# Performance work log

Measured on AMD Instinct MI355X. Metric: run time of the kernel, lower is better.

The kernel has to match this reference:

```python
import jax, jax.numpy as jnp
import numpy as np

B, S, D, H = 2, 2048, 1024, 16
DK = D // H
DFF = 4 * D
EPS = 1e-6


def layer_norm(x, gamma, beta):
    mu = jnp.mean(x, axis=-1, keepdims=True)
    var = jnp.mean(jnp.square(x - mu), axis=-1, keepdims=True)
    return (x - mu) * jax.lax.rsqrt(var + EPS) * gamma + beta


def setup_inputs() -> dict:
    key = jax.random.key(0)
    ks = jax.random.split(key, 10)
    xavier = (6.0 / (D + D)) ** 0.5
    kaiming = (6.0 / D) ** 0.5
    kaiming2 = (6.0 / DFF) ** 0.5
    return {
        "batch_X": jax.random.normal(ks[0], (B, S, D), dtype=jnp.float32),
        "padding_mask": jax.random.randint(ks[1], (B, S), 0, 2, dtype=jnp.int32),
        "W_Q": jax.random.uniform(ks[2], (D, D), jnp.float32, -xavier, xavier),
        "W_K": jax.random.uniform(ks[3], (D, D), jnp.float32, -xavier, xavier),
        "W_V": jax.random.uniform(ks[4], (D, D), jnp.float32, -xavier, xavier),
        "W_O": jax.random.uniform(ks[5], (D, D), jnp.float32, -xavier, xavier),
        "W1": jax.random.uniform(ks[6], (D, DFF), jnp.float32, -kaiming, kaiming),
        "b1": jnp.zeros((DFF,), jnp.float32),
        "W2": jax.random.uniform(ks[7], (DFF, D), jnp.float32, -kaiming2, kaiming2),
        "b2": jnp.zeros((D,), jnp.float32),
        "gamma1": jnp.ones((D,), jnp.float32),
        "beta1": jnp.zeros((D,), jnp.float32),
        "gamma2": jnp.ones((D,), jnp.float32),
        "beta2": jnp.zeros((D,), jnp.float32),
    }


def reference(batch_X, padding_mask, W_Q, W_K, W_V, W_O, W1, b1, W2, b2,
              gamma1, beta1, gamma2, beta2):
    x = batch_X
    b, s, d = x.shape

    # --- multi-head self-attention (use_mask=False: padding mask only) ---
    q = (x @ W_Q).reshape(b, s, H, DK)
    k = (x @ W_K).reshape(b, s, H, DK)
    v = (x @ W_V).reshape(b, s, H, DK)
    scores = jnp.einsum("bqhd,bkhd->bhqk", q, k) / jnp.sqrt(jnp.float32(DK))
    # mask[b,i,j] = (padding_mask[b,i] == 0) for all j: whole query rows are
    # either fully masked (softmax -> NaN -> zeroed in the original) or
    # fully unmasked. Equivalent math: softmax then zero padded query rows.
    probs = jax.nn.softmax(scores, axis=-1)
    keep = (padding_mask != 0).astype(probs.dtype)[:, None, :, None]  # [B,1,S,1]
    probs = probs * keep
    ctx = jnp.einsum("bhqk,bkhd->bqhd", probs, v).reshape(b, s, d)
    attn_out = ctx @ W_O

    # --- residual + LN (dropout identity in eval) ---
    x = x + layer_norm(attn_out, gamma1, beta1)

    # --- FFN ---
    h = jax.nn.relu(x @ W1 + b1)
    ffn_out = h @ W2 + b2
    x = x + layer_norm(ffn_out, gamma2, beta2)
    return x
```

## Files before the change

kernel.cpp:

```cpp
#include <hip/hip_runtime.h>

#define B 2
#define S 2048
#define D 1024
#define H 16
#define DKh 64
#define DFF 4096
#define M (B*S)

typedef unsigned short u16;
typedef unsigned int u32;
typedef __attribute__((ext_vector_type(8))) short short8;
typedef __attribute__((ext_vector_type(4))) float f32x4;

__device__ __forceinline__ u16 f2bf(float f) {
  union { float f; unsigned u; } v; v.f = f;
  unsigned r = v.u + 0x7fffu + ((v.u >> 16) & 1u);
  return (u16)(r >> 16);
}

__device__ __forceinline__ u32 pkbf(float a, float b) {
  union { float f; u32 u; } ua, ub; ua.f = a; ub.f = b;
  return ((ub.u + 0x8000u) & 0xffff0000u) | ((ua.u + 0x8000u) >> 16);
}

__device__ __forceinline__ void gload16(const void* g, void* l) {
  __builtin_amdgcn_global_load_lds((const __attribute__((address_space(1))) void*)g,
                                   (__attribute__((address_space(3))) void*)l, 16, 0, 0);
}

#define SBAR()  __builtin_amdgcn_sched_barrier(0)
#define WBAR()  __builtin_amdgcn_s_barrier()

__global__ __launch_bounds__(256) void cvtbf(const float* __restrict__ in,
                                             u16* __restrict__ out, int n4) {
  int i = blockIdx.x * 256 + threadIdx.x;
  if (i >= n4) return;
  float4 v = ((const float4*)in)[i];
  ushort4 o = make_ushort4(f2bf(v.x), f2bf(v.y), f2bf(v.z), f2bf(v.w));
  ((ushort4*)out)[i] = o;
}

__global__ __launch_bounds__(256) void tcvt(const float* __restrict__ W,
                                            u16* __restrict__ Wt, int K, int N) {
  __shared__ u16 l[64][65];
  const int n0 = blockIdx.x * 64, k0 = blockIdx.y * 64;
  const int tx = threadIdx.x & 63, ty = threadIdx.x >> 6;
#pragma unroll
  for (int j = 0; j < 16; ++j) {
    int r = j * 4 + ty;
    l[r][tx] = f2bf(W[(size_t)(k0 + r) * N + n0 + tx]);
  }
  __syncthreads();
#pragma unroll
  for (int j = 0; j < 16; ++j) {
    int r = j * 4 + ty;
    Wt[(size_t)(n0 + r) * K + k0 + tx] = l[tx][r];
  }
}

__global__ __launch_bounds__(256) void vtrans(const u16* __restrict__ V,
                                              u16* __restrict__ Vt, int ld) {
  __shared__ u16 l[64][65];
  const int s0 = blockIdx.x * 64, by = blockIdx.y;
  const int b = by >> 4, h = by & 15;
  const int tx = threadIdx.x & 63, ty = threadIdx.x >> 6;
#pragma unroll
  for (int j = 0; j < 16; ++j) {
    int r = j * 4 + ty;
    l[r][tx] = V[(size_t)(b * S + s0 + r) * ld + h * DKh + tx];
  }
  __syncthreads();
#pragma unroll
  for (int j = 0; j < 16; ++j) {
    int r = j * 4 + ty;
    Vt[(size_t)(by * 64 + r) * S + s0 + tx] = l[tx][r];
  }
}

template<int EPI>
__global__ __launch_bounds__(512, 2) void gemm256(const u16* __restrict__ Ag,
    const u16* __restrict__ Bg, void* __restrict__ Cout,
    const float* __restrict__ bias, int Mm, int N, int ld, int Kper) {
  __shared__ u16 lA[2 * 16384];
  __shared__ u16 lB[2 * 16384];
  const int t = threadIdx.x;
  const int lane = t & 63, w = t >> 6;
  const int wm = w >> 2, wn = w & 3;
  const int g = lane >> 4, c = lane & 15;
  const int swz = (c & 7) << 4;

  const int gx = gridDim.x, gy = gridDim.y;
  const int orig = blockIdx.y * gx + blockIdx.x;
  const int qchunk = (gx * gy) >> 3;
  const int wg = (orig & 7) * qchunk + (orig >> 3);
  const int bn0 = (wg % gx) * 256, bm0 = (wg / gx) * 256;
  const int koff = blockIdx.z * Kper;
  const int nk = Kper >> 6;

  f32x4 acc[8][4] = {};
  short8 af[4][2], bf[2][2];

  auto stageA = [&](int h, int buf, int kt) {
#pragma unroll
    for (int i = 0; i < 2; ++i) {
      int chunk = i * 512 + t;
      int rh = chunk >> 3;
      int cb = (chunk & 7) * 16;
      int r = (rh & 63) + (h + 2 * (rh >> 6)) * 64;
      gload16(Ag + (size_t)(bm0 + r) * ld + koff + kt * 64 + ((cb ^ ((r & 7) << 4)) >> 1),
              (void*)((char*)lA + buf * 32768 + h * 16384 + chunk * 16));
    }
  };
  auto stageB = [&](int h, int buf, int kt) {
#pragma unroll
    for (int i = 0; i < 2; ++i) {
      int chunk = i * 512 + t;
      int rh = chunk >> 3;
      int cb = (chunk & 7) * 16;
      int r = (rh & 31) + (h + 2 * (rh >> 5)) * 32;
      gload16(Bg + (size_t)(bn0 + r) * ld + koff + kt * 64 + ((cb ^ ((r & 7) << 4)) >> 1),
              (void*)((char*)lB + buf * 32768 + h * 16384 + chunk * 16));
    }
  };

#define RDA(mh) { const char* lab = (const char*)lA + cur * 32768;                          \
  _Pragma("unroll") for (int mt2 = 0; mt2 < 4; ++mt2)                                       \
    _Pragma("unroll") for (int kc = 0; kc < 2; ++kc)                                        \
      af[mt2][kc] = *(const short8*)(lab + (wm * 64 + (mh) * 128 + mt2 * 16 + c) * 128      \
                                         + ((kc * 64 + g * 16) ^ swz)); }
#define RDB(nh) { const char* lbb = (const char*)lB + cur * 32768;                          \
  _Pragma("unroll") for (int nt2 = 0; nt2 < 2; ++nt2)                                       \
    _Pragma("unroll") for (int kc = 0; kc < 2; ++kc)                                        \
      bf[nt2][kc] = *(const short8*)(lbb + ((nh) * 128 + wn * 32 + nt2 * 16 + c) * 128      \
                                         + ((kc * 64 + g * 16) ^ swz)); }
#define QMFMA(mh, nh) { __builtin_amdgcn_s_setprio(1);                                      \
  _Pragma("unroll") for (int mt2 = 0; mt2 < 4; ++mt2)                                       \
    _Pragma("unroll") for (int nt2 = 0; nt2 < 2; ++nt2)                                     \
      _Pragma("unroll") for (int kc = 0; kc < 2; ++kc)                                      \
        acc[(mh) * 4 + mt2][(nh) * 2 + nt2] = __builtin_amdgcn_mfma_f32_16x16x32_bf16(      \
            af[mt2][kc], bf[nt2][kc], acc[(mh) * 4 + mt2][(nh) * 2 + nt2], 0, 0, 0);        \
  __builtin_amdgcn_s_setprio(0); }

  stageA(0, 0, 0); stageB(0, 0, 0); stageA(1, 0, 0); stageB(1, 0, 0);
  asm volatile("s_waitcnt vmcnt(4)" ::: "memory");
  SBAR(); WBAR(); SBAR();

  int cur = 0;
  for (int kt = 0; kt < nk; ++kt) {
    const bool more = (kt + 1 < nk);
    RDB(0); RDA(0);
    if (more) { stageA(0, cur ^ 1, kt + 1);
                asm volatile("s_waitcnt vmcnt(4)" ::: "memory"); }
    else      { asm volatile("s_waitcnt vmcnt(2)" ::: "memory"); }
    SBAR(); WBAR(); SBAR();
    QMFMA(0, 0);
    SBAR(); WBAR(); SBAR();
    RDA(1);
    if (more) { stageB(0, cur ^ 1, kt + 1);
                asm volatile("s_waitcnt vmcnt(4)" ::: "memory"); }
    else      { asm volatile("s_waitcnt vmcnt(0)" ::: "memory"); }
    SBAR(); WBAR(); SBAR();
    QMFMA(1, 0);
    SBAR(); WBAR(); SBAR();
    RDB(1);
    if (more) stageA(1, cur ^ 1, kt + 1);
    SBAR(); WBAR(); SBAR();
    QMFMA(1, 1);
    SBAR(); WBAR(); SBAR();
    RDA(0);
    if (more) { stageB(1, cur ^ 1, kt + 1);
                asm volatile("s_waitcnt vmcnt(4)" ::: "memory"); }
    SBAR(); WBAR(); SBAR();
    QMFMA(0, 1);
    SBAR(); WBAR(); SBAR();
    cur ^= 1;
  }
#undef RDA
#undef RDB
#undef QMFMA

  float* plane = (EPI == 1) ? ((float*)Cout + (size_t)blockIdx.z * Mm * N) : (float*)Cout;
#pragma unroll
  for (int mt = 0; mt < 8; ++mt) {
#pragma unroll
    for (int nt = 0; nt < 4; ++nt) {
      const int col = bn0 + wn * 64 + nt * 16 + c;
      float bv = (EPI == 2) ? bias[col] : 0.0f;
#pragma unroll
      for (int r = 0; r < 4; ++r) {
        const int row = bm0 + wm * 128 + mt * 16 + g * 4 + r;
        float v = acc[mt][nt][r];
        if (EPI == 2) v = fmaxf(v + bv, 0.0f);
        if (EPI == 1) plane[(size_t)row * N + col] = v;
        else          ((u16*)Cout)[(size_t)row * N + col] = f2bf(v);
      }
    }
  }
}

__global__ __launch_bounds__(256) void attn_kernel(const u16* __restrict__ Q,
    const u16* __restrict__ Kp, const u16* __restrict__ Vt,
    const int* __restrict__ mask, u16* __restrict__ Ctx, int ldq) {
  __shared__ u16 lK[2][64 * 64];
  __shared__ u16 lV[2][64 * 64];
  __shared__ u16 lP[4 * 16 * 64];
  const int t = threadIdx.x, lane = t & 63, w = t >> 6;
  const int g = lane >> 4, c = lane & 15;
  const int gx = gridDim.x;
  const int orig = blockIdx.y * gx + blockIdx.x;
  const int qchunk = (gx * gridDim.y) >> 3;
  const int wg = (orig & 7) * qchunk + (orig >> 3);
  const int bx = wg % gx, by = wg / gx;
  const int b = by >> 4, h = by & 15;
  const int q0w = bx * 64 + w * 16;
  const float SCL = 0.18033688011112042f;

  short8 qf[2];
#pragma unroll
  for (int kc = 0; kc < 2; ++kc)
    qf[kc] = *(const short8*)&Q[(size_t)(b * S + q0w + c) * ldq + h * DKh + kc * 32 + g * 8];

  float lsum = 0.0f;
  f32x4 accO[4] = {};

  auto stage = [&](int buf, int it) {
    const int kv0 = it * 64;
#pragma unroll
    for (int q = 0; q < 2; ++q) {
      int idx = q * 256 + t;
      int row = idx >> 3;
      int colb = (idx & 7) * 16;
      int scol = colb ^ ((row & 7) << 4);
      gload16(Kp + (size_t)(b * S + kv0 + row) * ldq + h * DKh + scol / 2,
              (void*)(&lK[buf][0] + idx * 8));
      gload16(Vt + (size_t)(by * 64 + row) * S + kv0 + scol / 2,
              (void*)(&lV[buf][0] + idx * 8));
    }
  };

  stage(0, 0);
  int cur = 0;
  for (int it = 0; it < S / 64; ++it) {
    __syncthreads();
    if (it + 1 < S / 64) stage(cur ^ 1, it + 1);

    f32x4 sc[4];
#pragma unroll
    for (int ct = 0; ct < 4; ++ct) {
      f32x4 z = {0.f, 0.f, 0.f, 0.f};
#pragma unroll
      for (int kc = 0; kc < 2; ++kc) {
        int row = ct * 16 + c;
        int bcol = (kc * 64 + g * 16) ^ ((row & 7) << 4);
        short8 kf = *(const short8*)&lK[cur][row * 64 + bcol / 2];
        z = __builtin_amdgcn_mfma_f32_16x16x32_bf16(kf, qf[kc], z, 0, 0, 0);
      }
      sc[ct] = z;
    }

#pragma unroll
    for (int ct = 0; ct < 4; ++ct) {
      float p0 = __builtin_amdgcn_exp2f(sc[ct][0] * SCL);
      float p1 = __builtin_amdgcn_exp2f(sc[ct][1] * SCL);
      float p2 = __builtin_amdgcn_exp2f(sc[ct][2] * SCL);
      float p3 = __builtin_amdgcn_exp2f(sc[ct][3] * SCL);
      lsum += (p0 + p1) + (p2 + p3);
      uint2 pk;
      pk.x = pkbf(p0, p1);
      pk.y = pkbf(p2, p3);
      *(uint2*)&lP[w * 1024 + c * 64 + (((ct * 32 + g * 8) ^ ((c & 7) << 4)) >> 1)] = pk;
    }

    short8 pa[2];
#pragma unroll
    for (int kc = 0; kc < 2; ++kc)
      pa[kc] = *(const short8*)&lP[w * 1024 + c * 64 + (((kc * 64 + g * 16) ^ ((c & 7) << 4)) >> 1)];
#pragma unroll
    for (int dt = 0; dt < 4; ++dt) {
#pragma unroll
      for (int kc = 0; kc < 2; ++kc) {
        int rowV = dt * 16 + c;
        int bcolV = (kc * 64 + g * 16) ^ ((rowV & 7) << 4);
        short8 vb = *(const short8*)&lV[cur][rowV * 64 + bcolV / 2];
        accO[dt] = __builtin_amdgcn_mfma_f32_16x16x32_bf16(pa[kc], vb, accO[dt], 0, 0, 0);
      }
    }
    cur ^= 1;
  }

  lsum += __shfl_xor(lsum, 16);
  lsum += __shfl_xor(lsum, 32);

#pragma unroll
  for (int r = 0; r < 4; ++r) {
    int qrow = g * 4 + r;
    float lq = __shfl(lsum, qrow);
    int q = q0w + qrow;
    int keep = mask[b * S + q];
    float inv = (keep != 0) ? (1.0f / lq) : 0.0f;
#pragma unroll
    for (int dt = 0; dt < 4; ++dt) {
      float o = accO[dt][r] * inv;
      Ctx[(size_t)(b * S + q) * D + h * DKh + dt * 16 + c] = f2bf(o);
    }
  }
}

__global__ __launch_bounds__(256) void ln_res(const float* __restrict__ planes,
    int np, const float* __restrict__ bias, const float* __restrict__ Xres,
    const float* __restrict__ gamma, const float* __restrict__ beta,
    float* __restrict__ outF, u16* __restrict__ outB) {
  __shared__ float s1[4], s2[4];
  const int row = blockIdx.x, t = threadIdx.x;
  float4 y = ((const float4*)(planes + (size_t)row * D))[t];
  for (int j = 1; j < np; ++j) {
    const float4 y2 = ((const float4*)(planes + (size_t)j * M * D + (size_t)row * D))[t];
    y.x += y2.x; y.y += y2.y; y.z += y2.z; y.w += y2.w;
  }
  if (bias) {
    const float4 bb = ((const float4*)bias)[t];
    y.x += bb.x; y.y += bb.y; y.z += bb.z; y.w += bb.w;
  }
  float sm = y.x + y.y + y.z + y.w;
  float sq = y.x * y.x + y.y * y.y + y.z * y.z + y.w * y.w;
#pragma unroll
  for (int m2 = 1; m2 <= 32; m2 <<= 1) { sm += __shfl_xor(sm, m2); sq += __shfl_xor(sq, m2); }
  if ((t & 63) == 0) { s1[t >> 6] = sm; s2[t >> 6] = sq; }
  __syncthreads();
  float tot = s1[0] + s1[1] + s1[2] + s1[3];
  float tsq = s2[0] + s2[1] + s2[2] + s2[3];
  float mu = tot * (1.0f / D);
  float var = tsq * (1.0f / D) - mu * mu;
  float rstd = rsqrtf(var + 1e-6f);
  const float4 xr = ((const float4*)(Xres + (size_t)row * D))[t];
  const float4 ga = ((const float4*)gamma)[t];
  const float4 be = ((const float4*)beta)[t];
  float4 o;
  o.x = xr.x + (y.x - mu) * rstd * ga.x + be.x;
  o.y = xr.y + (y.y - mu) * rstd * ga.y + be.y;
  o.z = xr.z + (y.z - mu) * rstd * ga.z + be.z;
  o.w = xr.w + (y.w - mu) * rstd * ga.w + be.w;
  ((float4*)(outF + (size_t)row * D))[t] = o;
  if (outB) {
    ushort4 ob = make_ushort4(f2bf(o.x), f2bf(o.y), f2bf(o.z), f2bf(o.w));
    ((ushort4*)outB)[(size_t)row * (D / 4) + t] = ob;
  }
}

extern "C" void kernel_launch(void* const* d_in, const int* in_sizes, int n_in,
                              void* d_out, int out_size, void* d_ws, size_t ws_size,
                              hipStream_t stream) {
  const float* X   = (const float*)d_in[0];
  const int*   msk = (const int*)d_in[1];
  const float* WQ  = (const float*)d_in[2];
  const float* WK  = (const float*)d_in[3];
  const float* WV  = (const float*)d_in[4];
  const float* WO  = (const float*)d_in[5];
  const float* W1  = (const float*)d_in[6];
  const float* b1  = (const float*)d_in[7];
  const float* W2  = (const float*)d_in[8];
  const float* b2  = (const float*)d_in[9];
  const float* g1  = (const float*)d_in[10];
  const float* be1 = (const float*)d_in[11];
  const float* g2  = (const float*)d_in[12];
  const float* be2 = (const float*)d_in[13];
  float* out = (float*)d_out;

  char* ws = (char*)d_ws;
  size_t off = 0;
  auto alloc = [&](size_t bytes) {
    void* p = ws + off;
    off += (bytes + 1023) & ~(size_t)1023;
    return p;
  };
  u16* Xb     = (u16*)alloc((size_t)M * D * 2);
  u16* WQKVt  = (u16*)alloc((size_t)3 * D * D * 2);
  u16* WOt    = (u16*)alloc((size_t)D * D * 2);
  u16* W1t    = (u16*)alloc((size_t)DFF * D * 2);
  u16* W2t    = (u16*)alloc((size_t)D * DFF * 2);
  u16* QKVb   = (u16*)alloc((size_t)M * 3 * D * 2);
  u16* Vt     = (u16*)alloc((size_t)B * H * DKh * S * 2);
  u16* Ctx    = (u16*)alloc((size_t)M * D * 2);
  float* X1f  = (float*)alloc((size_t)M * D * 4);
  u16* X1b    = (u16*)alloc((size_t)M * D * 2);
  u16* Hb     = (u16*)alloc((size_t)M * DFF * 2);
  float* PP   = (float*)QKVb;
  if (off > ws_size) return;
  size_t off4 = off;
  float* PP4 = (float*)(ws + off4);
  off4 += (size_t)4 * M * D * 4;
  const bool split4 = (off4 <= ws_size);

  dim3 blk(256), blk5(512);

  cvtbf<<<dim3(M * D / 4 / 256), blk, 0, stream>>>(X, Xb, M * D / 4);
  tcvt<<<dim3(D / 64, D / 64), blk, 0, stream>>>(WQ, WQKVt + 0 * D * D, D, D);
  tcvt<<<dim3(D / 64, D / 64), blk, 0, stream>>>(WK, WQKVt + 1 * D * D, D, D);
  tcvt<<<dim3(D / 64, D / 64), blk, 0, stream>>>(WV, WQKVt + 2 * D * D, D, D);
  tcvt<<<dim3(D / 64, D / 64), blk, 0, stream>>>(WO, WOt, D, D);
  tcvt<<<dim3(DFF / 64, D / 64), blk, 0, stream>>>(W1, W1t, D, DFF);
  tcvt<<<dim3(D / 64, DFF / 64), blk, 0, stream>>>(W2, W2t, DFF, D);
  gemm256<0><<<dim3(3 * D / 256, M / 256), blk5, 0, stream>>>(Xb, WQKVt, QKVb, nullptr, M, 3 * D, D, D);
  vtrans<<<dim3(S / 64, B * H), blk, 0, stream>>>(QKVb + 2 * D, Vt, 3 * D);
  attn_kernel<<<dim3(S / 64, B * H), blk, 0, stream>>>(QKVb, QKVb + D, Vt, msk, Ctx, 3 * D);
  gemm256<1><<<dim3(D / 256, M / 256, 2), blk5, 0, stream>>>(Ctx, WOt, PP, nullptr, M, D, D, D / 2);
  ln_res<<<dim3(M), blk, 0, stream>>>(PP, 2, nullptr, X, g1, be1, X1f, X1b);
  gemm256<2><<<dim3(DFF / 256, M / 256), blk5, 0, stream>>>(X1b, W1t, Hb, b1, M, DFF, D, D);
  if (split4) {
    gemm256<1><<<dim3(D / 256, M / 256, 4), blk5, 0, stream>>>(Hb, W2t, PP4, nullptr, M, D, DFF, DFF / 4);
    ln_res<<<dim3(M), blk, 0, stream>>>(PP4, 4, b2, X1f, g2, be2, out, nullptr);
  } else {
    gemm256<1><<<dim3(D / 256, M / 256, 2), blk5, 0, stream>>>(Hb, W2t, PP, nullptr, M, D, DFF, DFF / 2);
    ln_res<<<dim3(M), blk, 0, stream>>>(PP, 2, b2, X1f, g2, be2, out, nullptr);
  }
}
```

Baseline: 265.6 us.

## Read K/V directly from global in attention, fold scale into Q GEMM

The attention kernel drops its double-buffered LDS staging of K and V. Each wave now loads its MFMA fragments straight from global memory (relying on cache), which removes the block-wide barriers and the LDS traffic. The softmax scale moves into the QKV GEMM epilogue for the Q columns, and the row-sum now comes from an MFMA against a vector of ones instead of scalar adds and shuffles. Packing to bf16 uses the hardware v_cvt_pk_bf16_f32 instruction. The risk is uncoalesced global loads and redundant K/V reads across the four waves, which may raise memory latency in the inner loop.

```diff
diff --git a/kernel.cpp b/kernel.cpp
--- a/kernel.cpp
+++ b/kernel.cpp
@@ -19,11 +19,6 @@
   return (u16)(r >> 16);
 }
 
-__device__ __forceinline__ u32 pkbf(float a, float b) {
-  union { float f; u32 u; } ua, ub; ua.f = a; ub.f = b;
-  return ((ub.u + 0x8000u) & 0xffff0000u) | ((ua.u + 0x8000u) >> 16);
-}
-
 __device__ __forceinline__ void gload16(const void* g, void* l) {
   __builtin_amdgcn_global_load_lds((const __attribute__((address_space(1))) void*)g,
                                    (__attribute__((address_space(3))) void*)l, 16, 0, 0);
@@ -81,7 +76,8 @@
 template<int EPI>
 __global__ __launch_bounds__(512, 2) void gemm256(const u16* __restrict__ Ag,
     const u16* __restrict__ Bg, void* __restrict__ Cout,
-    const float* __restrict__ bias, int Mm, int N, int ld, int Kper) {
+    const float* __restrict__ bias, int Mm, int N, int ld, int Kper,
+    int sCols, float qscl) {
   __shared__ u16 lA[2 * 16384];
   __shared__ u16 lB[2 * 16384];
   const int t = threadIdx.x;
@@ -192,6 +188,7 @@
         const int row = bm0 + wm * 128 + mt * 16 + g * 4 + r;
         float v = acc[mt][nt][r];
         if (EPI == 2) v = fmaxf(v + bv, 0.0f);
+        if (EPI == 0 && col < sCols) v *= qscl;
         if (EPI == 1) plane[(size_t)row * N + col] = v;
         else          ((u16*)Cout)[(size_t)row * N + col] = f2bf(v);
       }
@@ -202,8 +199,6 @@
 __global__ __launch_bounds__(256) void attn_kernel(const u16* __restrict__ Q,
     const u16* __restrict__ Kp, const u16* __restrict__ Vt,
     const int* __restrict__ mask, u16* __restrict__ Ctx, int ldq) {
-  __shared__ u16 lK[2][64 * 64];
-  __shared__ u16 lV[2][64 * 64];
   __shared__ u16 lP[4 * 16 * 64];
   const int t = threadIdx.x, lane = t & 63, w = t >> 6;
   const int g = lane >> 4, c = lane & 15;
@@ -214,36 +209,23 @@
   const int bx = wg % gx, by = wg / gx;
   const int b = by >> 4, h = by & 15;
   const int q0w = bx * 64 + w * 16;
-  const float SCL = 0.18033688011112042f;
 
   short8 qf[2];
 #pragma unroll
   for (int kc = 0; kc < 2; ++kc)
     qf[kc] = *(const short8*)&Q[(size_t)(b * S + q0w + c) * ldq + h * DKh + kc * 32 + g * 8];
 
-  float lsum = 0.0f;
+  const u16* Kb = Kp + (size_t)b * S * ldq + h * DKh;
+  const u16* Vb = Vt + (size_t)by * 64 * S;
+
   f32x4 accO[4] = {};
-
-  auto stage = [&](int buf, int it) {
+  f32x4 accL = {0.f, 0.f, 0.f, 0.f};
+  short8 ones8;
+#pragma unroll
+  for (int j = 0; j < 8; ++j) ones8[j] = (short)0x3F80;
+
+  for (int it = 0; it < S / 64; ++it) {
     const int kv0 = it * 64;
-#pragma unroll
-    for (int q = 0; q < 2; ++q) {
-      int idx = q * 256 + t;
-      int row = idx >> 3;
-      int colb = (idx & 7) * 16;
-      int scol = colb ^ ((row & 7) << 4);
-      gload16(Kp + (size_t)(b * S + kv0 + row) * ldq + h * DKh + scol / 2,
-              (void*)(&lK[buf][0] + idx * 8));
-      gload16(Vt + (size_t)(by * 64 + row) * S + kv0 + scol / 2,
-              (void*)(&lV[buf][0] + idx * 8));
-    }
-  };
-
-  stage(0, 0);
-  int cur = 0;
-  for (int it = 0; it < S / 64; ++it) {
-    __syncthreads();
-    if (it + 1 < S / 64) stage(cur ^ 1, it + 1);
 
     f32x4 sc[4];
 #pragma unroll
@@ -251,9 +233,7 @@
       f32x4 z = {0.f, 0.f, 0.f, 0.f};
 #pragma unroll
       for (int kc = 0; kc < 2; ++kc) {
-        int row = ct * 16 + c;
-        int bcol = (kc * 64 + g * 16) ^ ((row & 7) << 4);
-        short8 kf = *(const short8*)&lK[cur][row * 64 + bcol / 2];
+        short8 kf = *(const short8*)&Kb[(size_t)(kv0 + ct * 16 + c) * ldq + kc * 32 + g * 8];
         z = __builtin_amdgcn_mfma_f32_16x16x32_bf16(kf, qf[kc], z, 0, 0, 0);
       }
       sc[ct] = z;
@@ -261,14 +241,13 @@
 
 #pragma unroll
     for (int ct = 0; ct < 4; ++ct) {
-      float p0 = __builtin_amdgcn_exp2f(sc[ct][0] * SCL);
-      float p1 = __builtin_amdgcn_exp2f(sc[ct][1] * SCL);
-      float p2 = __builtin_amdgcn_exp2f(sc[ct][2] * SCL);
-      float p3 = __builtin_amdgcn_exp2f(sc[ct][3] * SCL);
-      lsum += (p0 + p1) + (p2 + p3);
+      float p0 = __builtin_amdgcn_exp2f(sc[ct][0]);
+      float p1 = __builtin_amdgcn_exp2f(sc[ct][1]);
+      float p2 = __builtin_amdgcn_exp2f(sc[ct][2]);
+      float p3 = __builtin_amdgcn_exp2f(sc[ct][3]);
       uint2 pk;
-      pk.x = pkbf(p0, p1);
-      pk.y = pkbf(p2, p3);
+      asm("v_cvt_pk_bf16_f32 %0, %1, %2" : "=v"(pk.x) : "v"(p0), "v"(p1));
+      asm("v_cvt_pk_bf16_f32 %0, %1, %2" : "=v"(pk.y) : "v"(p2), "v"(p3));
       *(uint2*)&lP[w * 1024 + c * 64 + (((ct * 32 + g * 8) ^ ((c & 7) << 4)) >> 1)] = pk;
     }
 
@@ -276,29 +255,24 @@
 #pragma unroll
     for (int kc = 0; kc < 2; ++kc)
       pa[kc] = *(const short8*)&lP[w * 1024 + c * 64 + (((kc * 64 + g * 16) ^ ((c & 7) << 4)) >> 1)];
+    accL = __builtin_amdgcn_mfma_f32_16x16x32_bf16(pa[0], ones8, accL, 0, 0, 0);
+    accL = __builtin_amdgcn_mfma_f32_16x16x32_bf16(pa[1], ones8, accL, 0, 0, 0);
+
 #pragma unroll
     for (int dt = 0; dt < 4; ++dt) {
 #pragma unroll
       for (int kc = 0; kc < 2; ++kc) {
-        int rowV = dt * 16 + c;
-        int bcolV = (kc * 64 + g * 16) ^ ((rowV & 7) << 4);
-        short8 vb = *(const short8*)&lV[cur][rowV * 64 + bcolV / 2];
+        short8 vb = *(const short8*)&Vb[(size_t)(dt * 16 + c) * S + kv0 + kc * 32 + g * 8];
         accO[dt] = __builtin_amdgcn_mfma_f32_16x16x32_bf16(pa[kc], vb, accO[dt], 0, 0, 0);
       }
     }
-    cur ^= 1;
-  }
-
-  lsum += __shfl_xor(lsum, 16);
-  lsum += __shfl_xor(lsum, 32);
+  }
 
 #pragma unroll
   for (int r = 0; r < 4; ++r) {
-    int qrow = g * 4 + r;
-    float lq = __shfl(lsum, qrow);
-    int q = q0w + qrow;
+    int q = q0w + g * 4 + r;
     int keep = mask[b * S + q];
-    float inv = (keep != 0) ? (1.0f / lq) : 0.0f;
+    float inv = (keep != 0) ? (1.0f / accL[r]) : 0.0f;
 #pragma unroll
     for (int dt = 0; dt < 4; ++dt) {
       float o = accO[dt][r] * inv;
@@ -366,6 +340,7 @@
   const float* g2  = (const float*)d_in[12];
   const float* be2 = (const float*)d_in[13];
   float* out = (float*)d_out;
+  const float SCL = 0.18033688011112042f;
 
   char* ws = (char*)d_ws;
   size_t off = 0;
@@ -401,17 +376,17 @@
   tcvt<<<dim3(D / 64, D / 64), blk, 0, stream>>>(WO, WOt, D, D);
   tcvt<<<dim3(DFF / 64, D / 64), blk, 0, stream>>>(W1, W1t, D, DFF);
   tcvt<<<dim3(D / 64, DFF / 64), blk, 0, stream>>>(W2, W2t, DFF, D);
-  gemm256<0><<<dim3(3 * D / 256, M / 256), blk5, 0, stream>>>(Xb, WQKVt, QKVb, nullptr, M, 3 * D, D, D);
+  gemm256<0><<<dim3(3 * D / 256, M / 256), blk5, 0, stream>>>(Xb, WQKVt, QKVb, nullptr, M, 3 * D, D, D, D, SCL);
   vtrans<<<dim3(S / 64, B * H), blk, 0, stream>>>(QKVb + 2 * D, Vt, 3 * D);
   attn_kernel<<<dim3(S / 64, B * H), blk, 0, stream>>>(QKVb, QKVb + D, Vt, msk, Ctx, 3 * D);
-  gemm256<1><<<dim3(D / 256, M / 256, 2), blk5, 0, stream>>>(Ctx, WOt, PP, nullptr, M, D, D, D / 2);
+  gemm256<1><<<dim3(D / 256, M / 256, 2), blk5, 0, stream>>>(Ctx, WOt, PP, nullptr, M, D, D, D / 2, 0, 1.0f);
   ln_res<<<dim3(M), blk, 0, stream>>>(PP, 2, nullptr, X, g1, be1, X1f, X1b);
-  gemm256<2><<<dim3(DFF / 256, M / 256), blk5, 0, stream>>>(X1b, W1t, Hb, b1, M, DFF, D, D);
+  gemm256<2><<<dim3(DFF / 256, M / 256), blk5, 0, stream>>>(X1b, W1t, Hb, b1, M, DFF, D, D, 0, 1.0f);
   if (split4) {
-    gemm256<1><<<dim3(D / 256, M / 256, 4), blk5, 0, stream>>>(Hb, W2t, PP4, nullptr, M, D, DFF, DFF / 4);
+    gemm256<1><<<dim3(D / 256, M / 256, 4), blk5, 0, stream>>>(Hb, W2t, PP4, nullptr, M, D, DFF, DFF / 4, 0, 1.0f);
     ln_res<<<dim3(M), blk, 0, stream>>>(PP4, 4, b2, X1f, g2, be2, out, nullptr);
   } else {
-    gemm256<1><<<dim3(D / 256, M / 256, 2), blk5, 0, stream>>>(Hb, W2t, PP, nullptr, M, D, DFF, DFF / 2);
+    gemm256<1><<<dim3(D / 256, M / 256, 2), blk5, 0, stream>>>(Hb, W2t, PP, nullptr, M, D, DFF, DFF / 2, 0, 1.0f);
     ln_res<<<dim3(M), blk, 0, stream>>>(PP, 2, b2, X1f, g2, be2, out, nullptr);
   }
 }
```

Measured after the change: 427.8 us. 61.0% more time.
